# Optimization experiments

Measured on AMD Instinct MI355X. Metric: run time of the kernel, lower is better.

## Reference

```python
import jax, jax.numpy as jnp
import numpy as np

B, T, IN, H, L, P = 512, 512, 1, 100, 4, 0.5  # batch, seq, input, hidden, layers, dropout


def setup_inputs() -> dict:
    key = jax.random.key(0)
    ks = jax.random.split(key, 12)
    k = 1.0 / np.sqrt(H)  # torch nn.LSTM init scale
    u = lambda kk, shape: jax.random.uniform(kk, shape, jnp.float32, -k, k)
    inp = {
        "x": jax.random.normal(ks[0], (B, T, IN), jnp.float32),
        "W_ih0": u(ks[1], (4 * H, IN)),          # layer 0 input weights
        "W_ih_rest": u(ks[2], (L - 1, 4 * H, H)),  # layers 1..3 input weights
        "W_hh": u(ks[3], (L, 4 * H, H)),
        "b_ih": u(ks[4], (L, 4 * H)),
        "b_hh": u(ks[5], (L, 4 * H)),
        "W_out": u(ks[6], (1, H)),
        "b_out": u(ks[7], (1,)),
        # inter-layer dropout keep-masks (torch applies dropout to outputs of layers 0..L-2)
        "drop_masks": jax.random.bernoulli(ks[8], 1.0 - P, (L - 1, B, T, H)).astype(jnp.float32),
    }
    return inp


def _lstm_layer(seq, Wih, Whh, b):
    # seq: [T, B, in_dim]; returns [T, B, H]. PyTorch gate order: i, f, g, o.
    h0 = jnp.zeros((seq.shape[1], Whh.shape[-1]), seq.dtype)

    def step(carry, xt):
        h, c = carry
        gates = xt @ Wih.T + h @ Whh.T + b  # [B, 4H]
        i, f, g, o = jnp.split(gates, 4, axis=-1)
        c = jax.nn.sigmoid(f) * c + jax.nn.sigmoid(i) * jnp.tanh(g)
        h = jax.nn.sigmoid(o) * jnp.tanh(c)
        return (h, c), h

    _, hs = jax.lax.scan(step, (h0, h0), seq)
    return hs


def reference(x, W_ih0, W_ih_rest, W_hh, b_ih, b_hh, W_out, b_out, drop_masks):
    scale = 1.0 / (1.0 - P)
    seq = jnp.swapaxes(x, 0, 1)  # [T, B, IN] (batch_first -> time-major)
    seq = _lstm_layer(seq, W_ih0, W_hh[0], b_ih[0] + b_hh[0])
    for l in range(1, L):
        seq = seq * (jnp.swapaxes(drop_masks[l - 1], 0, 1) * scale)
        seq = _lstm_layer(seq, W_ih_rest[l - 1], W_hh[l], b_ih[l] + b_hh[l])
    last = seq[-1]  # [B, H] == lstm_out[:, -1]
    return last @ W_out.T + b_out  # [B, 1]
```

## Files before the change

### kernel.cpp

```cpp
#include <hip/hip_runtime.h>
#include <cstdint>
#include <cstddef>

#define BB 512
#define TT 512
#define HH 100
#define G4 400

template<bool IS_L0, bool WRITE_DROP>
__global__ __launch_bounds__(448, 2)
void rec_kernel(const float* __restrict__ x,
                const float* __restrict__ xc,
                const float* __restrict__ Whh_l,
                const float* __restrict__ Wih0,
                const float* __restrict__ bih_l,
                const float* __restrict__ bhh_l,
                const float* __restrict__ dmask_l,
                float* __restrict__ hdrop,
                float* __restrict__ st_h,
                float* __restrict__ st_c)
{
    __shared__ float hbuf[2][2][112];
    __shared__ float gsh[2][400];

    const int tid = threadIdx.x;
    const int p   = tid >> 1;
    const int e   = tid & 1;
    const bool rowok = (p < 200);
    const int pc  = rowok ? p : 199;
    const int r0  = pc;
    const int r1  = pc + 200;
    const int b   = blockIdx.x * 2 + e;

    float wf0[100], wf1[100];
    {
        const float4* w0 = (const float4*)(Whh_l + (size_t)r0 * HH);
        const float4* w1 = (const float4*)(Whh_l + (size_t)r1 * HH);
        #pragma unroll
        for (int m = 0; m < 25; ++m) {
            ((float4*)wf0)[m] = w0[m];
            ((float4*)wf1)[m] = w1[m];
        }
    }

    float wx0 = 0.f, wx1 = 0.f, bs0 = 0.f, bs1 = 0.f;
    if (IS_L0) {
        wx0 = Wih0[r0];  bs0 = bih_l[r0] + bhh_l[r0];
        wx1 = Wih0[r1];  bs1 = bih_l[r1] + bhh_l[r1];
    }

    ((float*)hbuf)[tid] = 0.f;

    const bool p2 = (p < HH);
    const int jj  = p2 ? p : 0;
    float c2 = 0.f, hlast = 0.f;

    __syncthreads();

    float gin0 = 0.f, gin1 = 0.f, xv = 0.f, mk = 0.f;
    if (IS_L0) {
        xv = x[(size_t)b * TT];
    } else {
        gin0 = xc[(size_t)b * G4 + r0];
        gin1 = xc[(size_t)b * G4 + r1];
    }
    if (WRITE_DROP && p2) mk = dmask_l[(size_t)b * TT * HH + jj];

    int cur = 0;
    for (int t = 0; t < TT; ++t) {
        const int tn = (t + 1 < TT) ? (t + 1) : t;

        float nxv = 0.f, ngin0 = 0.f, ngin1 = 0.f, nmk = 0.f;
        if (IS_L0) {
            nxv = x[(size_t)b * TT + tn];
        } else {
            const size_t base = (size_t)tn * BB * G4 + (size_t)b * G4;
            ngin0 = xc[base + r0];
            ngin1 = xc[base + r1];
        }
        if (WRITE_DROP && p2) nmk = dmask_l[((size_t)b * TT + tn) * HH + jj];

        if (IS_L0) {
            gin0 = fmaf(xv, wx0, bs0);
            gin1 = fmaf(xv, wx1, bs1);
        }

        float a0 = 0.f, a0b = 0.f, a1 = 0.f, a1b = 0.f;
        {
            const float4* hp = (const float4*)&hbuf[cur][e][0];
            #pragma unroll
            for (int m = 0; m < 25; ++m) {
                const float4 hv = hp[m];
                a0  = fmaf(wf0[4 * m + 0], hv.x, a0);
                a0b = fmaf(wf0[4 * m + 1], hv.y, a0b);
                a0  = fmaf(wf0[4 * m + 2], hv.z, a0);
                a0b = fmaf(wf0[4 * m + 3], hv.w, a0b);
                a1  = fmaf(wf1[4 * m + 0], hv.x, a1);
                a1b = fmaf(wf1[4 * m + 1], hv.y, a1b);
                a1  = fmaf(wf1[4 * m + 2], hv.z, a1);
                a1b = fmaf(wf1[4 * m + 3], hv.w, a1b);
            }
        }
        if (rowok) {
            gsh[e][pc]       = a0 + a0b + gin0;
            gsh[e][pc + 200] = a1 + a1b + gin1;
        }
        __syncthreads();

        const int nxt = cur ^ 1;
        if (p2) {
            const float gi = gsh[e][jj];
            const float gf = gsh[e][HH + jj];
            const float gg = gsh[e][2 * HH + jj];
            const float go = gsh[e][3 * HH + jj];
            const float i_ = 1.f / (1.f + __expf(-gi));
            const float f_ = 1.f / (1.f + __expf(-gf));
            const float o_ = 1.f / (1.f + __expf(-go));
            const float gt = 1.f - 2.f / (__expf(gg + gg) + 1.f);
            c2 = fmaf(f_, c2, i_ * gt);
            const float th = 1.f - 2.f / (__expf(c2 + c2) + 1.f);
            const float h = o_ * th;
            hlast = h;
            hbuf[nxt][e][jj] = h;
            if (WRITE_DROP)
                hdrop[((size_t)t * BB + b) * HH + jj] = h * mk * 2.f;
        }
        __syncthreads();
        cur = nxt;
        gin0 = ngin0; gin1 = ngin1;
        xv = nxv; mk = nmk;
    }

    if (p2) {
        st_h[(size_t)b * HH + jj] = hlast;
        st_c[(size_t)b * HH + jj] = c2;
    }
}

__global__ __launch_bounds__(256, 2)
void xc_gemm(const float* __restrict__ A,
             const float* __restrict__ W,
             const float* __restrict__ bih_l,
             const float* __restrict__ bhh_l,
             float* __restrict__ xc)
{
    __shared__ float At[HH][132];
    __shared__ float Bt[HH][68];

    const int tid = threadIdx.x;
    const int n0  = blockIdx.x * 64;
    const size_t m0 = (size_t)blockIdx.y * 128;

    for (int s = tid; s < 128 * 25; s += 256) {
        const int r = s / 25, kq = s - r * 25;
        const float4 v = *(const float4*)&A[(m0 + r) * HH + kq * 4];
        At[kq * 4 + 0][r] = v.x; At[kq * 4 + 1][r] = v.y;
        At[kq * 4 + 2][r] = v.z; At[kq * 4 + 3][r] = v.w;
    }
    for (int s = tid; s < 64 * 25; s += 256) {
        const int r = s / 25, kq = s - r * 25;
        const int col = n0 + r;
        float4 v = {0.f, 0.f, 0.f, 0.f};
        if (col < G4) v = *(const float4*)&W[(size_t)col * HH + kq * 4];
        Bt[kq * 4 + 0][r] = v.x; Bt[kq * 4 + 1][r] = v.y;
        Bt[kq * 4 + 2][r] = v.z; Bt[kq * 4 + 3][r] = v.w;
    }
    __syncthreads();

    const int tx = tid & 15;
    const int ty = tid >> 4;
    float acc[8][4];
    #pragma unroll
    for (int i = 0; i < 8; ++i)
        #pragma unroll
        for (int j = 0; j < 4; ++j) acc[i][j] = 0.f;

    #pragma unroll 4
    for (int k = 0; k < HH; ++k) {
        const float4 a0 = *(const float4*)&At[k][ty * 8];
        const float4 a1 = *(const float4*)&At[k][ty * 8 + 4];
        const float4 bv = *(const float4*)&Bt[k][tx * 4];
        const float av[8] = {a0.x, a0.y, a0.z, a0.w, a1.x, a1.y, a1.z, a1.w};
        #pragma unroll
        for (int i = 0; i < 8; ++i) {
            acc[i][0] = fmaf(av[i], bv.x, acc[i][0]);
            acc[i][1] = fmaf(av[i], bv.y, acc[i][1]);
            acc[i][2] = fmaf(av[i], bv.z, acc[i][2]);
            acc[i][3] = fmaf(av[i], bv.w, acc[i][3]);
        }
    }

    const int col = n0 + tx * 4;
    if (col < G4) {
        const float4 u = *(const float4*)&bih_l[col];
        const float4 v = *(const float4*)&bhh_l[col];
        const float4 bias = {u.x + v.x, u.y + v.y, u.z + v.z, u.w + v.w};
        #pragma unroll
        for (int i = 0; i < 8; ++i) {
            const size_t r = m0 + ty * 8 + i;
            float4 o = {acc[i][0] + bias.x, acc[i][1] + bias.y,
                        acc[i][2] + bias.z, acc[i][3] + bias.w};
            *(float4*)&xc[r * G4 + col] = o;
        }
    }
}

__global__ __launch_bounds__(256)
void out_kernel(const float* __restrict__ st_h3,
                const float* __restrict__ Wout,
                const float* __restrict__ bout,
                float* __restrict__ out)
{
    const int b = blockIdx.x * 256 + threadIdx.x;
    if (b < BB) {
        float sum = bout[0];
        #pragma unroll 4
        for (int k = 0; k < HH; ++k)
            sum = fmaf(st_h3[(size_t)b * HH + k], Wout[k], sum);
        out[b] = sum;
    }
}

extern "C" void kernel_launch(void* const* d_in, const int* in_sizes, int n_in,
                              void* d_out, int out_size, void* d_ws, size_t ws_size,
                              hipStream_t stream)
{
    const float* x     = (const float*)d_in[0];
    const float* Wih0  = (const float*)d_in[1];
    const float* WihR  = (const float*)d_in[2];
    const float* Whh   = (const float*)d_in[3];
    const float* bih   = (const float*)d_in[4];
    const float* bhh   = (const float*)d_in[5];
    const float* Wout  = (const float*)d_in[6];
    const float* bout  = (const float*)d_in[7];
    const float* dmask = (const float*)d_in[8];
    float* out = (float*)d_out;

    float* ws    = (float*)d_ws;
    float* xcb   = ws;
    float* hdrop = xcb + (size_t)TT * BB * G4;
    float* sth   = hdrop + (size_t)TT * BB * HH;
    float* stc   = sth + (size_t)4 * BB * HH;

    const dim3 rgrid(BB / 2), rblk(448);
    const dim3 ggrid(7, (TT * BB) / 128), gblk(256);

    rec_kernel<true, true><<<rgrid, rblk, 0, stream>>>(
        x, nullptr, Whh, Wih0, bih, bhh, dmask,
        hdrop, sth, stc);
    for (int l = 1; l < 4; ++l) {
        xc_gemm<<<ggrid, gblk, 0, stream>>>(
            hdrop, WihR + (size_t)(l - 1) * G4 * HH,
            bih + l * G4, bhh + l * G4, xcb);
        if (l < 3) {
            rec_kernel<false, true><<<rgrid, rblk, 0, stream>>>(
                nullptr, xcb, Whh + (size_t)l * G4 * HH,
                nullptr, nullptr, nullptr,
                dmask + (size_t)l * BB * TT * HH,
                hdrop, sth + (size_t)l * BB * HH, stc + (size_t)l * BB * HH);
        } else {
            rec_kernel<false, false><<<rgrid, rblk, 0, stream>>>(
                nullptr, xcb, Whh + (size_t)l * G4 * HH,
                nullptr, nullptr, nullptr,
                nullptr,
                nullptr, sth + (size_t)l * BB * HH, stc + (size_t)l * BB * HH);
        }
    }
    out_kernel<<<dim3(2), dim3(256), 0, stream>>>(sth + (size_t)3 * BB * HH, Wout, bout, out);
}
```

Before: 4.155 ms.

## Pair gate rows per thread so cell update uses a lane shuffle instead of a barrier

Each thread pair now owns all four gate rows of one hidden unit (i/g on one lane, f/o on the other), computes the activations locally, and exchanges the i*g product with a lane shuffle. This drops the gate shared-memory round trip and one __syncthreads per timestep. The weights are staged through a large shared buffer for coalesced loading and held as float4 registers, and launch bounds drop to one block per CU. The large static shared allocation and higher register pressure may limit occupancy.

```diff
diff --git a/kernel.cpp b/kernel.cpp
--- a/kernel.cpp
+++ b/kernel.cpp
@@ -8,7 +8,7 @@
 #define G4 400
 
 template<bool IS_L0, bool WRITE_DROP>
-__global__ __launch_bounds__(448, 2)
+__global__ __launch_bounds__(448, 1)
 void rec_kernel(const float* __restrict__ x,
                 const float* __restrict__ xc,
                 const float* __restrict__ Whh_l,
@@ -20,28 +20,36 @@
                 float* __restrict__ st_h,
                 float* __restrict__ st_c)
 {
-    __shared__ float hbuf[2][2][112];
-    __shared__ float gsh[2][400];
-
-    const int tid = threadIdx.x;
-    const int p   = tid >> 1;
-    const int e   = tid & 1;
-    const bool rowok = (p < 200);
-    const int pc  = rowok ? p : 199;
-    const int r0  = pc;
-    const int r1  = pc + 200;
-    const int b   = blockIdx.x * 2 + e;
-
-    float wf0[100], wf1[100];
+    __shared__ float sh[G4 * HH];
+
+    const int tid  = threadIdx.x;
+    const int e    = (tid < 224) ? 0 : 1;
+    const int off  = tid - e * 224;
+    const int j    = off >> 1;
+    const int role = off & 1;
+    const bool active = (j < HH);
+    const int jc   = active ? j : (HH - 1);
+    const int r0   = role * 100 + jc;
+    const int r1   = r0 + 200;
+    const int b    = blockIdx.x * 2 + e;
+
     {
-        const float4* w0 = (const float4*)(Whh_l + (size_t)r0 * HH);
-        const float4* w1 = (const float4*)(Whh_l + (size_t)r1 * HH);
-        #pragma unroll
-        for (int m = 0; m < 25; ++m) {
-            ((float4*)wf0)[m] = w0[m];
-            ((float4*)wf1)[m] = w1[m];
-        }
-    }
+        const float4* src = (const float4*)Whh_l;
+        float4* dst = (float4*)sh;
+        for (int i = tid; i < G4 * HH / 4; i += 448) dst[i] = src[i];
+    }
+    __syncthreads();
+
+    float4 wf0[25], wf1[25];
+    {
+        const float4* s0 = (const float4*)&sh[r0 * HH];
+        const float4* s1 = (const float4*)&sh[r1 * HH];
+        #pragma unroll
+        for (int m = 0; m < 25; ++m) { wf0[m] = s0[m]; wf1[m] = s1[m]; }
+    }
+    __syncthreads();
+
+    for (int i = tid; i < G4 * HH; i += 448) sh[i] = 0.f;
 
     float wx0 = 0.f, wx1 = 0.f, bs0 = 0.f, bs1 = 0.f;
     if (IS_L0) {
@@ -49,10 +57,7 @@
         wx1 = Wih0[r1];  bs1 = bih_l[r1] + bhh_l[r1];
     }
 
-    ((float*)hbuf)[tid] = 0.f;
-
-    const bool p2 = (p < HH);
-    const int jj  = p2 ? p : 0;
+    const bool isB = (role == 1);
     float c2 = 0.f, hlast = 0.f;
 
     __syncthreads();
@@ -64,7 +69,7 @@
         gin0 = xc[(size_t)b * G4 + r0];
         gin1 = xc[(size_t)b * G4 + r1];
     }
-    if (WRITE_DROP && p2) mk = dmask_l[(size_t)b * TT * HH + jj];
+    if (WRITE_DROP && isB && active) mk = dmask_l[(size_t)b * TT * HH + jc];
 
     int cur = 0;
     for (int t = 0; t < TT; ++t) {
@@ -74,11 +79,12 @@
         if (IS_L0) {
             nxv = x[(size_t)b * TT + tn];
         } else {
-            const size_t base = (size_t)tn * BB * G4 + (size_t)b * G4;
+            const size_t base = (size_t)tn * (BB * G4) + (size_t)b * G4;
             ngin0 = xc[base + r0];
             ngin1 = xc[base + r1];
         }
-        if (WRITE_DROP && p2) nmk = dmask_l[((size_t)b * TT + tn) * HH + jj];
+        if (WRITE_DROP && isB && active)
+            nmk = dmask_l[((size_t)b * TT + tn) * HH + jc];
 
         if (IS_L0) {
             gin0 = fmaf(xv, wx0, bs0);
@@ -87,53 +93,52 @@
 
         float a0 = 0.f, a0b = 0.f, a1 = 0.f, a1b = 0.f;
         {
-            const float4* hp = (const float4*)&hbuf[cur][e][0];
+            const float4* hp = (const float4*)&sh[cur * 224 + e * 112];
             #pragma unroll
             for (int m = 0; m < 25; ++m) {
                 const float4 hv = hp[m];
-                a0  = fmaf(wf0[4 * m + 0], hv.x, a0);
-                a0b = fmaf(wf0[4 * m + 1], hv.y, a0b);
-                a0  = fmaf(wf0[4 * m + 2], hv.z, a0);
-                a0b = fmaf(wf0[4 * m + 3], hv.w, a0b);
-                a1  = fmaf(wf1[4 * m + 0], hv.x, a1);
-                a1b = fmaf(wf1[4 * m + 1], hv.y, a1b);
-                a1  = fmaf(wf1[4 * m + 2], hv.z, a1);
-                a1b = fmaf(wf1[4 * m + 3], hv.w, a1b);
+                a0  = fmaf(wf0[m].x, hv.x, a0);
+                a0b = fmaf(wf0[m].y, hv.y, a0b);
+                a0  = fmaf(wf0[m].z, hv.z, a0);
+                a0b = fmaf(wf0[m].w, hv.w, a0b);
+                a1  = fmaf(wf1[m].x, hv.x, a1);
+                a1b = fmaf(wf1[m].y, hv.y, a1b);
+                a1  = fmaf(wf1[m].z, hv.z, a1);
+                a1b = fmaf(wf1[m].w, hv.w, a1b);
             }
         }
-        if (rowok) {
-            gsh[e][pc]       = a0 + a0b + gin0;
-            gsh[e][pc + 200] = a1 + a1b + gin1;
-        }
-        __syncthreads();
+        const float pre0 = a0 + a0b + gin0;
+        const float pre1 = a1 + a1b + gin1;
+
+        const float s0 = 1.f / (1.f + __expf(-pre0));
+        const float E1 = __expf(isB ? (-pre1) : (pre1 + pre1));
+        const float rr = 1.f / (1.f + E1);
+        const float s1 = isB ? rr : fmaf(-2.f, rr, 1.f);
+
+        const float pv   = s0 * s1;
+        const float recv = __shfl_xor(pv, 1);
 
         const int nxt = cur ^ 1;
-        if (p2) {
-            const float gi = gsh[e][jj];
-            const float gf = gsh[e][HH + jj];
-            const float gg = gsh[e][2 * HH + jj];
-            const float go = gsh[e][3 * HH + jj];
-            const float i_ = 1.f / (1.f + __expf(-gi));
-            const float f_ = 1.f / (1.f + __expf(-gf));
-            const float o_ = 1.f / (1.f + __expf(-go));
-            const float gt = 1.f - 2.f / (__expf(gg + gg) + 1.f);
-            c2 = fmaf(f_, c2, i_ * gt);
-            const float th = 1.f - 2.f / (__expf(c2 + c2) + 1.f);
-            const float h = o_ * th;
+        if (isB) {
+            c2 = fmaf(s0, c2, recv);
+            const float Ec = __expf(c2 + c2);
+            const float th = 1.f - 2.f / (Ec + 1.f);
+            const float h  = s1 * th;
             hlast = h;
-            hbuf[nxt][e][jj] = h;
-            if (WRITE_DROP)
-                hdrop[((size_t)t * BB + b) * HH + jj] = h * mk * 2.f;
+            if (active) {
+                sh[nxt * 224 + e * 112 + j] = h;
+                if (WRITE_DROP)
+                    hdrop[((size_t)t * BB + b) * HH + j] = h * mk * 2.f;
+            }
         }
         __syncthreads();
         cur = nxt;
-        gin0 = ngin0; gin1 = ngin1;
-        xv = nxv; mk = nmk;
-    }
-
-    if (p2) {
-        st_h[(size_t)b * HH + jj] = hlast;
-        st_c[(size_t)b * HH + jj] = c2;
+        gin0 = ngin0; gin1 = ngin1; xv = nxv; mk = nmk;
+    }
+
+    if (isB && active) {
+        st_h[(size_t)b * HH + j] = hlast;
+        st_c[(size_t)b * HH + j] = c2;
     }
 }
 
```

New measurement: 3.578 ms. -13.9%, faster.
